# Kernel optimization log

Hardware: AMD Instinct MI355X
Metric: run time of the kernel (lower is better)

The kernel has to match this reference:

```python
import jax, jax.numpy as jnp
import numpy as np

EMBED = 1024
ATTN = 1024
HEADS = 16
HEAD_DIM = ATTN // HEADS


def setup_inputs() -> dict:
    key = jax.random.key(0)
    ks = jax.random.split(key, 8)
    s = 1.0 / np.sqrt(EMBED)
    sa = 1.0 / np.sqrt(ATTN)
    return {
        "queries": jax.random.normal(ks[0], (4, 512, EMBED), jnp.float32),
        "context": jax.random.normal(ks[1], (4, 2048, EMBED), jnp.float32),
        "Wq": jax.random.normal(ks[2], (EMBED, ATTN), jnp.float32) * s,
        "bq": jnp.zeros((ATTN,), jnp.float32),
        "Wkv": jax.random.normal(ks[3], (EMBED, 2 * ATTN), jnp.float32) * s,
        "bkv": jnp.zeros((2 * ATTN,), jnp.float32),
        "Wo": jax.random.normal(ks[4], (ATTN, EMBED), jnp.float32) * sa,
        "bo": jnp.zeros((EMBED,), jnp.float32),
    }


def reference(queries, context, Wq, bq, Wkv, bkv, Wo, bo):
    B, Lq, _ = queries.shape
    Lk = context.shape[1]
    q = queries @ Wq + bq                      # [B, Lq, ATTN]
    kv = context @ Wkv + bkv                   # [B, Lk, 2*ATTN]
    k, v = jnp.split(kv, 2, axis=-1)
    q = q.reshape(B, Lq, HEADS, HEAD_DIM)
    k = k.reshape(B, Lk, HEADS, HEAD_DIM)
    v = v.reshape(B, Lk, HEADS, HEAD_DIM)
    scale = 1.0 / np.sqrt(HEAD_DIM)
    scores = jnp.einsum("bqhd,bkhd->bhqk", q, k) * scale
    attn = jax.nn.softmax(scores, axis=-1)
    x = jnp.einsum("bhqk,bkhd->bqhd", attn, v).reshape(B, Lq, ATTN)
    return x @ Wo + bo
```

## Files before the change

### kernel.cpp

```cpp
#include <hip/hip_runtime.h>
#include <hip/hip_bf16.h>
#include <stdint.h>

typedef unsigned short u16;
typedef __attribute__((ext_vector_type(8))) __bf16 bf16x8;
typedef __attribute__((ext_vector_type(2))) __bf16 bf16x2;
typedef __attribute__((ext_vector_type(4))) float f32x4;
typedef __attribute__((ext_vector_type(4))) u16 u16x4;
typedef __attribute__((ext_vector_type(4))) float f32x4v;

typedef __attribute__((address_space(1))) void gvoid_t;
typedef __attribute__((address_space(3))) void lvoid_t;

#define BAR()    asm volatile("s_barrier" ::: "memory")
#define WAITV0() asm volatile("s_waitcnt vmcnt(0)" ::: "memory")
#define WAITV2() asm volatile("s_waitcnt vmcnt(2)" ::: "memory")
#define WAITV4() asm volatile("s_waitcnt vmcnt(4)" ::: "memory")
#define WAITV8() asm volatile("s_waitcnt vmcnt(8)" ::: "memory")

__device__ inline u16 f2bf(float f) {
    uint32_t u = __float_as_uint(f);
    u += 0x7fff + ((u >> 16) & 1);
    return (u16)(u >> 16);
}

__device__ inline float bf2f(u16 v) {
    return __uint_as_float(((uint32_t)v) << 16);
}

__device__ inline void gll16(const void* g, void* l) {
    __builtin_amdgcn_global_load_lds((gvoid_t*)g, (lvoid_t*)l, 16, 0, 0);
}

__device__ inline f32x4 mfma16(bf16x8 a, bf16x8 b, f32x4 c) {
    return __builtin_amdgcn_mfma_f32_16x16x32_bf16(a, b, c, 0, 0, 0);
}

__device__ inline int vslot(int r) {
    int n = r >> 4;
    return ((n >> 1) << 5) + (((r >> 2) & 3) << 3) + ((n & 1) << 2) + (r & 3);
}

__global__ __launch_bounds__(256) void prep_kernel(
        const float* __restrict__ q, const float* __restrict__ c,
        const float* __restrict__ Wq, const float* __restrict__ Wkv,
        const float* __restrict__ Wo, u16* __restrict__ qb,
        u16* __restrict__ cb, u16* __restrict__ WqT,
        u16* __restrict__ WkvT, u16* __restrict__ WoT) {
    const int bid = blockIdx.x;
    const int tid = threadIdx.x;
    if (bid < 10240) {
        int i = bid * 256 + tid;
        const float* src; u16* dst; int j;
        if (i < 524288) { src = q; dst = qb; j = i; }
        else            { src = c; dst = cb; j = i - 524288; }
        f32x4v f = ((const f32x4v*)src)[j];
        u16x4 o;
        o[0] = f2bf(f[0]); o[1] = f2bf(f[1]); o[2] = f2bf(f[2]); o[3] = f2bf(f[3]);
        ((u16x4*)dst)[j] = o;
        return;
    }
    int b2 = bid - 10240;
    const float* W; u16* WT; int N, n0, k0;
    if (b2 < 1024)      { W = Wq;  WT = WqT;  N = 1024; n0 = (b2 & 31) * 32; k0 = (b2 >> 5) * 32; }
    else if (b2 < 3072) { int b3 = b2 - 1024; W = Wkv; WT = WkvT; N = 2048; n0 = (b3 & 63) * 32; k0 = (b3 >> 6) * 32; }
    else                { int b3 = b2 - 3072; W = Wo;  WT = WoT;  N = 1024; n0 = (b3 & 31) * 32; k0 = (b3 >> 5) * 32; }
    __shared__ float t[32][33];
    int x = tid & 31, y = tid >> 5;
    for (int yy = y; yy < 32; yy += 8)
        t[yy][x] = W[(size_t)(k0 + yy) * N + n0 + x];
    __syncthreads();
    for (int yy = y; yy < 32; yy += 8)
        WT[(size_t)(n0 + yy) * 1024 + k0 + x] = f2bf(t[x][yy]);
}

template <int MODE>
__global__ __launch_bounds__(512, 2) void gemm_bt(
        const u16* __restrict__ A, const u16* __restrict__ Bt,
        const float* __restrict__ bias, int M, int N, int K,
        float scale, void* __restrict__ out0) {
    __shared__ u16 lds[4][6144];
    const int NT = K >> 5;
    const int tid = threadIdx.x;
    const int lane = tid & 63, wv = tid >> 6;
    const int c16 = lane & 15, g = lane >> 4;
    const int m0 = blockIdx.y * 64, n0 = blockIdx.x * 128;

    const int idxA = (wv & 3) * 64 + lane;
    const int rA = idxA >> 2, ccA = (idxA & 3) ^ ((rA >> 1) & 3);
    const size_t offA = (size_t)(m0 + rA) * K + ccA * 8;
    const int dstA = (wv & 3) * 512;
    const int idxB = wv * 64 + lane;
    const int rB = idxB >> 2, ccB = (idxB & 3) ^ ((rB >> 1) & 3);
    const size_t offB = (size_t)(n0 + rB) * K + ccB * 8;
    const int dstB = 2048 + wv * 512;

    auto stage = [&](int t) {
        gll16(A + offA + t * 32, &lds[t & 3][dstA]);
        gll16(Bt + offB + t * 32, &lds[t & 3][dstB]);
    };

    const int wm = (wv >> 1) * 16, wn = (wv & 1) * 64;
    f32x4 acc[4] = {};

    auto compute = [&](int slot) {
        const u16* la = &lds[slot][0];
        const u16* lb = &lds[slot][2048];
        int rowa = wm + c16;
        bf16x8 af = *(const bf16x8*)&la[rowa * 32 + (g ^ ((rowa >> 1) & 3)) * 8];
        bf16x8 bfr[4];
#pragma unroll
        for (int n = 0; n < 4; n++) {
            int row = wn + n * 16 + c16;
            bfr[n] = *(const bf16x8*)&lb[row * 32 + (g ^ ((row >> 1) & 3)) * 8];
        }
        __builtin_amdgcn_s_setprio(1);
#pragma unroll
        for (int n = 0; n < 4; n++)
            acc[n] = mfma16(af, bfr[n], acc[n]);
        __builtin_amdgcn_s_setprio(0);
    };

    stage(0); stage(1); stage(2);

    for (int t = 0; t < NT - 2; ++t) {
        WAITV4();
        BAR();
        if (t + 3 < NT) stage(t + 3);
        compute(t & 3);
    }
    WAITV2(); BAR(); compute((NT - 2) & 3);
    WAITV0(); BAR(); compute((NT - 1) & 3);

#pragma unroll
    for (int n = 0; n < 4; n++) {
        int col = n0 + wn + n * 16 + c16;
        float bv = bias[col];
        int rowb = m0 + wm + g * 4;
#pragma unroll
        for (int j = 0; j < 4; j++) {
            float v = (acc[n][j] + bv) * scale;
            int row = rowb + j;
            if (MODE == 0) {
                ((u16*)out0)[(size_t)row * N + col] = f2bf(v);
            } else {
                ((float*)out0)[(size_t)row * N + col] = v;
            }
        }
    }
}

__global__ __launch_bounds__(512, 2) void fused_qkv(
        const u16* __restrict__ cb, const u16* __restrict__ WkvT,
        const float* __restrict__ bkv, u16* __restrict__ Kp,
        u16* __restrict__ VpT,
        const u16* __restrict__ qb, const u16* __restrict__ WqT,
        const float* __restrict__ bq, float qscale, u16* __restrict__ Qp) {
    __shared__ u16 smem[4][2][8192];
    const int tid = threadIdx.x;
    const int lane = tid & 63, wv = tid >> 6;
    const int c16 = lane & 15, g = lane >> 4;
    const int bidg = blockIdx.x;

    if (bidg < 256) {
        const int K = 1024, NT = 32;
        const int cpx = 32;
        const int sw = (bidg & 7) * cpx + (bidg >> 3);
        const int bx = sw & 7, by = sw >> 3;
        const int m0 = by * 256, n0 = bx * 256;

        const int isB = wv >> 2;
        const int rbase = (wv & 3) * 64;
        const u16* src = isB ? WkvT : cb;
        const int base0 = isB ? n0 : m0;
        size_t off[4];
        const u16* ldst[4];
#pragma unroll
        for (int i = 0; i < 4; i++) {
            int rl = rbase + i * 16 + (lane >> 2);
            int ch = (lane & 3) ^ ((rl >> 1) & 3);
            off[i] = (size_t)(base0 + rl) * K + ch * 8;
            ldst[i] = &smem[0][0][0] + ((size_t)isB * 256 * 32) + (size_t)(rbase + i * 16) * 32;
        }
        const size_t slotStride = 2 * 256 * 32;

        auto stage = [&](int t) {
            const u16* s0 = src + (size_t)t * 32;
            u16* d = (u16*)ldst[0] + (size_t)(t & 3) * slotStride;
            gll16(s0 + off[0], d);
            gll16(s0 + off[1], d + 16 * 32);
            gll16(s0 + off[2], d + 32 * 32);
            gll16(s0 + off[3], d + 48 * 32);
        };

        const int wm = wv >> 2;
        const int wn = wv & 3;
        f32x4 acc[8][4] = {};

        auto compute = [&](int slot) {
            const u16* la = &smem[slot][0][0];
            const u16* lb = &smem[slot][1][0];
            bf16x8 af[8], bfr[4];
#pragma unroll
            for (int m = 0; m < 8; m++) {
                int row = wm * 128 + m * 16 + c16;
                af[m] = *(const bf16x8*)&la[row * 32 + (g ^ ((row >> 1) & 3)) * 8];
            }
#pragma unroll
            for (int n = 0; n < 4; n++) {
                int row = wn * 64 + n * 16 + c16;
                bfr[n] = *(const bf16x8*)&lb[row * 32 + (g ^ ((row >> 1) & 3)) * 8];
            }
            __builtin_amdgcn_s_setprio(1);
#pragma unroll
            for (int m = 0; m < 8; m++)
#pragma unroll
                for (int n = 0; n < 4; n++)
                    acc[m][n] = mfma16(af[m], bfr[n], acc[m][n]);
            __builtin_amdgcn_s_setprio(0);
        };

        stage(0); stage(1); stage(2);

        for (int t = 0; t < NT - 2; ++t) {
            WAITV8();
            BAR();
            if (t + 3 < NT) stage(t + 3);
            compute(t & 3);
        }
        WAITV4(); BAR(); compute((NT - 2) & 3);
        WAITV0(); BAR(); compute((NT - 1) & 3);

        const bool isV = (n0 >= 1024);
#pragma unroll
        for (int n = 0; n < 4; n++) {
            int col = n0 + wn * 64 + n * 16 + c16;
            float bv = bkv[col];
#pragma unroll
            for (int m = 0; m < 8; m++) {
                int rowb = m0 + wm * 128 + m * 16 + g * 4;
                if (isV) {
                    u16x4 pk;
#pragma unroll
                    for (int j = 0; j < 4; j++) pk[j] = f2bf(acc[m][n][j] + bv);
                    int vcol = (rowb & ~63) + vslot(rowb & 63);
                    *(u16x4*)&VpT[(size_t)(col - 1024) * 8192 + vcol] = pk;
                } else {
#pragma unroll
                    for (int j = 0; j < 4; j++)
                        Kp[(size_t)(rowb + j) * 1024 + col] = f2bf(acc[m][n][j] + bv);
                }
            }
        }
    } else {
        const int K = 1024, N = 1024, NT = 32;
        const int b2 = bidg - 256;
        const int m0 = (b2 >> 3) * 64, n0 = (b2 & 7) * 128;
        u16* base = &smem[0][0][0];

        const int idxA = (wv & 3) * 64 + lane;
        const int rA = idxA >> 2, ccA = (idxA & 3) ^ ((rA >> 1) & 3);
        const size_t offA = (size_t)(m0 + rA) * K + ccA * 8;
        const int dstA = (wv & 3) * 512;
        const int idxB = wv * 64 + lane;
        const int rB = idxB >> 2, ccB = (idxB & 3) ^ ((rB >> 1) & 3);
        const size_t offB = (size_t)(n0 + rB) * K + ccB * 8;
        const int dstB = 2048 + wv * 512;

        auto stage = [&](int t) {
            u16* d = base + (t & 3) * 6144;
            gll16(qb + offA + t * 32, d + dstA);
            gll16(WqT + offB + t * 32, d + dstB);
        };

        const int wm = (wv >> 1) * 16, wn = (wv & 1) * 64;
        f32x4 acc[4] = {};

        auto compute = [&](int slot) {
            const u16* la = base + slot * 6144;
            const u16* lb = la + 2048;
            int rowa = wm + c16;
            bf16x8 af = *(const bf16x8*)&la[rowa * 32 + (g ^ ((rowa >> 1) & 3)) * 8];
            bf16x8 bfr[4];
#pragma unroll
            for (int n = 0; n < 4; n++) {
                int row = wn + n * 16 + c16;
                bfr[n] = *(const bf16x8*)&lb[row * 32 + (g ^ ((row >> 1) & 3)) * 8];
            }
            __builtin_amdgcn_s_setprio(1);
#pragma unroll
            for (int n = 0; n < 4; n++)
                acc[n] = mfma16(af, bfr[n], acc[n]);
            __builtin_amdgcn_s_setprio(0);
        };

        stage(0); stage(1); stage(2);

        for (int t = 0; t < NT - 2; ++t) {
            WAITV4();
            BAR();
            if (t + 3 < NT) stage(t + 3);
            compute(t & 3);
        }
        WAITV2(); BAR(); compute((NT - 2) & 3);
        WAITV0(); BAR(); compute((NT - 1) & 3);

#pragma unroll
        for (int n = 0; n < 4; n++) {
            int col = n0 + wn + n * 16 + c16;
            float bv = bq[col];
            int rowb = m0 + wm + g * 4;
#pragma unroll
            for (int j = 0; j < 4; j++) {
                float v = (acc[n][j] + bv) * qscale;
                Qp[(size_t)(rowb + j) * N + col] = f2bf(v);
            }
        }
    }
}

__global__ __launch_bounds__(256, 3) void attn_split_kernel(
        const u16* __restrict__ Qp, const u16* __restrict__ Kp,
        const u16* __restrict__ VpT, u16* __restrict__ Opart,
        float* __restrict__ ml) {
    __shared__ u16 lKV[3][2][64 * 64];
    const int NT = 16;
    const int tid = threadIdx.x;
    const int lane = tid & 63, wv = tid >> 6;
    const int c16 = lane & 15, g = lane >> 4;
    const int bid = blockIdx.x;
    const int qblk = bid >> 7;
    const int low = bid & 127;
    const int h = low & 15, z = low >> 4;
    const int b = z >> 1, sp = z & 1;
    const int kvbase = sp * 1024;

    bf16x8 qf[2][2];
#pragma unroll
    for (int qs = 0; qs < 2; qs++) {
        int qrow = b * 512 + qblk * 128 + qs * 64 + wv * 16 + c16;
        qf[qs][0] = *(const bf16x8*)(Qp + (size_t)qrow * 1024 + h * 64 + g * 8);
        qf[qs][1] = *(const bf16x8*)(Qp + (size_t)qrow * 1024 + h * 64 + 32 + g * 8);
    }

    f32x4 acc[2][4] = {};
    float m_s[2] = {-1e30f, -1e30f}, l_s[2] = {0.f, 0.f};

    const int r0 = tid >> 3, c0 = (tid & 7) ^ (r0 & 7);
    const int r1 = 32 + r0,  c1 = (tid & 7) ^ (r1 & 7);
    const int dst0 = wv * 512, dst1 = 2048 + wv * 512;

    auto stageKV = [&](int t) {
        int slot = t % 3;
        int kv0 = kvbase + t * 64;
        u16* dK = &lKV[slot][0][0];
        u16* dV = &lKV[slot][1][0];
        gll16(Kp + (size_t)(b * 2048 + kv0 + r0) * 1024 + h * 64 + c0 * 8, dK + dst0);
        gll16(Kp + (size_t)(b * 2048 + kv0 + r1) * 1024 + h * 64 + c1 * 8, dK + dst1);
        gll16(VpT + (size_t)(h * 64 + r0) * 8192 + b * 2048 + kv0 + c0 * 8, dV + dst0);
        gll16(VpT + (size_t)(h * 64 + r1) * 8192 + b * 2048 + kv0 + c1 * 8, dV + dst1);
    };

    stageKV(0); stageKV(1);
    for (int t = 0; t < NT; ++t) {
        if (t < NT - 1) { WAITV4(); } else { WAITV0(); }
        BAR();
        if (t + 2 < NT) stageKV(t + 2);

        const int slot = t % 3;
        const u16* lK = &lKV[slot][0][0];
        const u16* lV = &lKV[slot][1][0];

        f32x4 s[2][4];
#pragma unroll
        for (int n = 0; n < 4; n++) {
            s[0][n] = f32x4{0.f, 0.f, 0.f, 0.f};
            s[1][n] = f32x4{0.f, 0.f, 0.f, 0.f};
        }
        __builtin_amdgcn_s_setprio(1);
#pragma unroll
        for (int n = 0; n < 4; n++) {
            int key = n * 16 + c16;
#pragma unroll
            for (int kk = 0; kk < 2; kk++) {
                bf16x8 kf = *(const bf16x8*)&lK[key * 64 + (((kk * 4 + g) ^ (key & 7))) * 8];
                s[0][n] = mfma16(kf, qf[0][kk], s[0][n]);
                s[1][n] = mfma16(kf, qf[1][kk], s[1][n]);
            }
        }
        __builtin_amdgcn_s_setprio(0);

        uint32_t r[2][4][2];
#pragma unroll
        for (int qs = 0; qs < 2; qs++) {
            float mn0 = fmaxf(fmaxf(s[qs][0][0], s[qs][0][1]), fmaxf(s[qs][0][2], s[qs][0][3]));
            float mn1 = fmaxf(fmaxf(s[qs][1][0], s[qs][1][1]), fmaxf(s[qs][1][2], s[qs][1][3]));
            float mn2 = fmaxf(fmaxf(s[qs][2][0], s[qs][2][1]), fmaxf(s[qs][2][2], s[qs][2][3]));
            float mn3 = fmaxf(fmaxf(s[qs][3][0], s[qs][3][1]), fmaxf(s[qs][3][2], s[qs][3][3]));
            float mx = fmaxf(fmaxf(mn0, mn1), fmaxf(mn2, mn3));
            mx = fmaxf(mx, __shfl_xor(mx, 16));
            mx = fmaxf(mx, __shfl_xor(mx, 32));

            if (!__all(mx - m_s[qs] <= 8.0f)) {
                float mn = fmaxf(m_s[qs], mx);
                float al = exp2f(m_s[qs] - mn);
                m_s[qs] = mn;
                l_s[qs] *= al;
                float alr[4];
#pragma unroll
                for (int j = 0; j < 4; j++) alr[j] = __shfl(al, g * 4 + j);
#pragma unroll
                for (int nd = 0; nd < 4; nd++)
#pragma unroll
                    for (int j = 0; j < 4; j++) acc[qs][nd][j] *= alr[j];
            }

            float sums[4];
#pragma unroll
            for (int n = 0; n < 4; n++) {
                float p0 = exp2f(s[qs][n][0] - m_s[qs]);
                float p1 = exp2f(s[qs][n][1] - m_s[qs]);
                float p2 = exp2f(s[qs][n][2] - m_s[qs]);
                float p3 = exp2f(s[qs][n][3] - m_s[qs]);
                sums[n] = (p0 + p1) + (p2 + p3);
                union { bf16x2 h; uint32_t u; } ca, cb;
                ca.h[0] = (__bf16)p0; ca.h[1] = (__bf16)p1;
                cb.h[0] = (__bf16)p2; cb.h[1] = (__bf16)p3;
                r[qs][n][0] = ca.u; r[qs][n][1] = cb.u;
            }
            float sum = (sums[0] + sums[1]) + (sums[2] + sums[3]);
            sum += __shfl_xor(sum, 16);
            sum += __shfl_xor(sum, 32);
            l_s[qs] += sum;
        }

        __builtin_amdgcn_s_setprio(1);
#pragma unroll
        for (int kk2 = 0; kk2 < 2; kk2++) {
            union { bf16x8 v8; uint32_t u[4]; } pa0, pa1;
            pa0.u[0] = r[0][kk2 * 2][0];     pa0.u[1] = r[0][kk2 * 2][1];
            pa0.u[2] = r[0][kk2 * 2 + 1][0]; pa0.u[3] = r[0][kk2 * 2 + 1][1];
            pa1.u[0] = r[1][kk2 * 2][0];     pa1.u[1] = r[1][kk2 * 2][1];
            pa1.u[2] = r[1][kk2 * 2 + 1][0]; pa1.u[3] = r[1][kk2 * 2 + 1][1];
#pragma unroll
            for (int nd = 0; nd < 4; nd++) {
                int d = nd * 16 + c16;
                bf16x8 vf = *(const bf16x8*)&lV[d * 64 + (((kk2 * 4 + g) ^ (d & 7))) * 8];
                acc[0][nd] = mfma16(pa0.v8, vf, acc[0][nd]);
                acc[1][nd] = mfma16(pa1.v8, vf, acc[1][nd]);
            }
        }
        __builtin_amdgcn_s_setprio(0);
    }

#pragma unroll
    for (int qs = 0; qs < 2; qs++) {
#pragma unroll
        for (int j = 0; j < 4; j++) {
            int rowq = b * 512 + qblk * 128 + qs * 64 + wv * 16 + g * 4 + j;
            size_t idx = (size_t)sp * 32768 + (size_t)rowq * 16 + h;
#pragma unroll
            for (int nd = 0; nd < 4; nd++)
                Opart[idx * 64 + nd * 16 + c16] = f2bf(acc[qs][nd][j]);
        }
        if (g == 0) {
            int rowq = b * 512 + qblk * 128 + qs * 64 + wv * 16 + c16;
            size_t idx = (size_t)sp * 32768 + (size_t)rowq * 16 + h;
            ml[idx * 2] = m_s[qs];
            ml[idx * 2 + 1] = l_s[qs];
        }
    }
}

__global__ __launch_bounds__(256) void attn_combine_kernel(
        const u16* __restrict__ Opart, const float* __restrict__ ml,
        u16* __restrict__ X) {
    const int tid = threadIdx.x;
    const int r = blockIdx.x * 4 + (tid >> 6);
    const int d = tid & 63;
    float m0 = ml[(size_t)r * 2], l0 = ml[(size_t)r * 2 + 1];
    float m1 = ml[(size_t)(32768 + r) * 2], l1 = ml[(size_t)(32768 + r) * 2 + 1];
    float M = fmaxf(m0, m1);
    float a0 = exp2f(m0 - M), a1 = exp2f(m1 - M);
    float li = 1.f / (l0 * a0 + l1 * a1);
    float o0 = bf2f(Opart[(size_t)r * 64 + d]);
    float o1 = bf2f(Opart[(size_t)(32768 + r) * 64 + d]);
    float o = (o0 * a0 + o1 * a1) * li;
    int qrow = r >> 4, h = r & 15;
    X[(size_t)qrow * 1024 + h * 64 + d] = f2bf(o);
}

extern "C" void kernel_launch(void* const* d_in, const int* in_sizes, int n_in,
                              void* d_out, int out_size, void* d_ws, size_t ws_size,
                              hipStream_t stream) {
    const float* queries = (const float*)d_in[0];
    const float* context = (const float*)d_in[1];
    const float* Wq      = (const float*)d_in[2];
    const float* bq      = (const float*)d_in[3];
    const float* Wkv     = (const float*)d_in[4];
    const float* bkv     = (const float*)d_in[5];
    const float* Wo      = (const float*)d_in[6];
    const float* bo      = (const float*)d_in[7];

    char* ws = (char*)d_ws;
    u16* qb   = (u16*)(ws);
    u16* cb   = (u16*)(ws + (4ull  << 20));
    u16* WqT  = (u16*)(ws + (20ull << 20));
    u16* WkvT = (u16*)(ws + (22ull << 20));
    u16* WoT  = (u16*)(ws + (26ull << 20));
    u16* Qp   = (u16*)(ws + (28ull << 20));
    u16* Kp   = (u16*)(ws + (32ull << 20));
    u16* VpT  = (u16*)(ws + (48ull << 20));
    u16* X    = (u16*)(ws + (64ull << 20));
    float* ml    = (float*)qb;
    u16*   Opart = (u16*)cb;

    prep_kernel<<<dim3(14336), dim3(256), 0, stream>>>(queries, context, Wq, Wkv, Wo,
                                                       qb, cb, WqT, WkvT, WoT);

    fused_qkv<<<dim3(512), dim3(512), 0, stream>>>(cb, WkvT, bkv, Kp, VpT,
                                                   qb, WqT, bq, 0.18033688f, Qp);
    attn_split_kernel<<<dim3(512), dim3(256), 0, stream>>>(Qp, Kp, VpT, Opart, ml);
    attn_combine_kernel<<<dim3(8192), dim3(256), 0, stream>>>(Opart, ml, X);
    gemm_bt<2><<<dim3(8, 32), dim3(512), 0, stream>>>(X, WoT, bo, 2048, 1024, 1024,
                                                      1.0f, d_out);
}
```

Baseline: 117.8 us.

## Fuse context fp32-to-bf16 conversion into KV projection GEMM loads

The separate prep pass that converted the fp32 context to bf16 is removed. The KV GEMM now reads fp32 context directly into registers, converts it to bf16 and writes it into LDS, while the weight tiles still use direct global-to-LDS loads. The pipeline is restructured with register double buffering (even/odd) and adjusted vmcnt/lgkmcnt waits. This saves a full write and re-read of the bf16 context buffer. In exchange the GEMM moves twice as many bytes for its A operand, uses more registers, and does conversion ALU work inside the main loop.

```diff
diff --git a/kernel.cpp b/kernel.cpp
--- a/kernel.cpp
+++ b/kernel.cpp
@@ -12,11 +12,14 @@
 typedef __attribute__((address_space(1))) void gvoid_t;
 typedef __attribute__((address_space(3))) void lvoid_t;
 
-#define BAR()    asm volatile("s_barrier" ::: "memory")
-#define WAITV0() asm volatile("s_waitcnt vmcnt(0)" ::: "memory")
-#define WAITV2() asm volatile("s_waitcnt vmcnt(2)" ::: "memory")
-#define WAITV4() asm volatile("s_waitcnt vmcnt(4)" ::: "memory")
-#define WAITV8() asm volatile("s_waitcnt vmcnt(8)" ::: "memory")
+#define BAR()     asm volatile("s_barrier" ::: "memory")
+#define WAITV0()  asm volatile("s_waitcnt vmcnt(0)" ::: "memory")
+#define WAITV2()  asm volatile("s_waitcnt vmcnt(2)" ::: "memory")
+#define WAITV4()  asm volatile("s_waitcnt vmcnt(4)" ::: "memory")
+#define WAITV6()  asm volatile("s_waitcnt vmcnt(6)" ::: "memory")
+#define WAITV8()  asm volatile("s_waitcnt vmcnt(8)" ::: "memory")
+#define WAITV12() asm volatile("s_waitcnt vmcnt(12)" ::: "memory")
+#define WAITLGKM0() asm volatile("s_waitcnt lgkmcnt(0)" ::: "memory")
 
 __device__ inline u16 f2bf(float f) {
     uint32_t u = __float_as_uint(f);
@@ -42,25 +45,21 @@
 }
 
 __global__ __launch_bounds__(256) void prep_kernel(
-        const float* __restrict__ q, const float* __restrict__ c,
-        const float* __restrict__ Wq, const float* __restrict__ Wkv,
-        const float* __restrict__ Wo, u16* __restrict__ qb,
-        u16* __restrict__ cb, u16* __restrict__ WqT,
+        const float* __restrict__ q, const float* __restrict__ Wq,
+        const float* __restrict__ Wkv, const float* __restrict__ Wo,
+        u16* __restrict__ qb, u16* __restrict__ WqT,
         u16* __restrict__ WkvT, u16* __restrict__ WoT) {
     const int bid = blockIdx.x;
     const int tid = threadIdx.x;
-    if (bid < 10240) {
+    if (bid < 2048) {
         int i = bid * 256 + tid;
-        const float* src; u16* dst; int j;
-        if (i < 524288) { src = q; dst = qb; j = i; }
-        else            { src = c; dst = cb; j = i - 524288; }
-        f32x4v f = ((const f32x4v*)src)[j];
+        f32x4v f = ((const f32x4v*)q)[i];
         u16x4 o;
         o[0] = f2bf(f[0]); o[1] = f2bf(f[1]); o[2] = f2bf(f[2]); o[3] = f2bf(f[3]);
-        ((u16x4*)dst)[j] = o;
+        ((u16x4*)qb)[i] = o;
         return;
     }
-    int b2 = bid - 10240;
+    int b2 = bid - 2048;
     const float* W; u16* WT; int N, n0, k0;
     if (b2 < 1024)      { W = Wq;  WT = WqT;  N = 1024; n0 = (b2 & 31) * 32; k0 = (b2 >> 5) * 32; }
     else if (b2 < 3072) { int b3 = b2 - 1024; W = Wkv; WT = WkvT; N = 2048; n0 = (b3 & 63) * 32; k0 = (b3 >> 6) * 32; }
@@ -151,7 +150,7 @@
 }
 
 __global__ __launch_bounds__(512, 2) void fused_qkv(
-        const u16* __restrict__ cb, const u16* __restrict__ WkvT,
+        const float* __restrict__ ctx, const u16* __restrict__ WkvT,
         const float* __restrict__ bkv, u16* __restrict__ Kp,
         u16* __restrict__ VpT,
         const u16* __restrict__ qb, const u16* __restrict__ WqT,
@@ -169,28 +168,42 @@
         const int bx = sw & 7, by = sw >> 3;
         const int m0 = by * 256, n0 = bx * 256;
 
-        const int isB = wv >> 2;
-        const int rbase = (wv & 3) * 64;
-        const u16* src = isB ? WkvT : cb;
-        const int base0 = isB ? n0 : m0;
-        size_t off[4];
-        const u16* ldst[4];
-#pragma unroll
-        for (int i = 0; i < 4; i++) {
-            int rl = rbase + i * 16 + (lane >> 2);
-            int ch = (lane & 3) ^ ((rl >> 1) & 3);
-            off[i] = (size_t)(base0 + rl) * K + ch * 8;
-            ldst[i] = &smem[0][0][0] + ((size_t)isB * 256 * 32) + (size_t)(rbase + i * 16) * 32;
-        }
-        const size_t slotStride = 2 * 256 * 32;
-
-        auto stage = [&](int t) {
-            const u16* s0 = src + (size_t)t * 32;
-            u16* d = (u16*)ldst[0] + (size_t)(t & 3) * slotStride;
-            gll16(s0 + off[0], d);
-            gll16(s0 + off[1], d + 16 * 32);
-            gll16(s0 + off[2], d + 32 * 32);
-            gll16(s0 + off[3], d + 48 * 32);
+        const int rA0 = tid >> 2,         chA0 = (tid & 3) ^ ((rA0 >> 1) & 3);
+        const int rA1 = (tid + 512) >> 2, chA1 = (tid & 3) ^ ((rA1 >> 1) & 3);
+        const size_t offA0 = (size_t)(m0 + rA0) * K + chA0 * 8;
+        const size_t offA1 = (size_t)(m0 + rA1) * K + chA1 * 8;
+        const int dA0 = tid * 8, dA1 = (tid + 512) * 8;
+        size_t offB[2]; int dstB[2];
+#pragma unroll
+        for (int j = 0; j < 2; j++) {
+            int cch = j * 512 + wv * 64 + lane;
+            int r = cch >> 2, ch = (cch & 3) ^ ((r >> 1) & 3);
+            offB[j] = (size_t)(n0 + r) * K + ch * 8;
+            dstB[j] = (j * 512 + wv * 64) * 8;
+        }
+
+        f32x4v raE[4], raO[4];
+        auto loadA = [&](int t, f32x4v* ra) {
+            ra[0] = *(const f32x4v*)(ctx + offA0 + (size_t)t * 32);
+            ra[1] = *(const f32x4v*)(ctx + offA0 + (size_t)t * 32 + 4);
+            ra[2] = *(const f32x4v*)(ctx + offA1 + (size_t)t * 32);
+            ra[3] = *(const f32x4v*)(ctx + offA1 + (size_t)t * 32 + 4);
+        };
+        auto writeA = [&](int t, const f32x4v* ra) {
+            u16* d = &smem[t & 3][0][0];
+            union { u16 s[8]; bf16x8 v; } p0, p1;
+#pragma unroll
+            for (int j = 0; j < 4; j++) {
+                p0.s[j] = f2bf(ra[0][j]); p0.s[4 + j] = f2bf(ra[1][j]);
+                p1.s[j] = f2bf(ra[2][j]); p1.s[4 + j] = f2bf(ra[3][j]);
+            }
+            *(bf16x8*)(d + dA0) = p0.v;
+            *(bf16x8*)(d + dA1) = p1.v;
+        };
+        auto stageB = [&](int t) {
+#pragma unroll
+            for (int j = 0; j < 2; j++)
+                gll16(WkvT + offB[j] + (size_t)t * 32, &smem[t & 3][1][0] + dstB[j]);
         };
 
         const int wm = wv >> 2;
@@ -220,16 +233,26 @@
             __builtin_amdgcn_s_setprio(0);
         };
 
-        stage(0); stage(1); stage(2);
-
-        for (int t = 0; t < NT - 2; ++t) {
-            WAITV8();
+        loadA(0, raE); stageB(0);
+        loadA(1, raO); stageB(1);
+        writeA(0, raE);
+        loadA(2, raE); stageB(2);
+        writeA(1, raO);
+
+        for (int t = 0; t < NT; ++t) {
+            if (t < NT - 2) { WAITV12(); } else if (t == NT - 2) { WAITV6(); } else { WAITV0(); }
+            WAITLGKM0();
             BAR();
-            if (t + 3 < NT) stage(t + 3);
+            if (t & 1) {
+                if (t + 3 < NT) loadA(t + 3, raE);
+                if (t + 2 < NT) writeA(t + 2, raO);
+            } else {
+                if (t + 3 < NT) loadA(t + 3, raO);
+                if (t + 2 < NT) writeA(t + 2, raE);
+            }
+            if (t + 3 < NT) stageB(t + 3);
             compute(t & 3);
         }
-        WAITV4(); BAR(); compute((NT - 2) & 3);
-        WAITV0(); BAR(); compute((NT - 1) & 3);
 
         const bool isV = (n0 >= 1024);
 #pragma unroll
@@ -504,7 +527,6 @@
 
     char* ws = (char*)d_ws;
     u16* qb   = (u16*)(ws);
-    u16* cb   = (u16*)(ws + (4ull  << 20));
     u16* WqT  = (u16*)(ws + (20ull << 20));
     u16* WkvT = (u16*)(ws + (22ull << 20));
     u16* WoT  = (u16*)(ws + (26ull << 20));
@@ -513,12 +535,12 @@
     u16* VpT  = (u16*)(ws + (48ull << 20));
     u16* X    = (u16*)(ws + (64ull << 20));
     float* ml    = (float*)qb;
-    u16*   Opart = (u16*)cb;
-
-    prep_kernel<<<dim3(14336), dim3(256), 0, stream>>>(queries, context, Wq, Wkv, Wo,
-                                                       qb, cb, WqT, WkvT, WoT);
-
-    fused_qkv<<<dim3(512), dim3(512), 0, stream>>>(cb, WkvT, bkv, Kp, VpT,
+    u16*   Opart = (u16*)(ws + (4ull << 20));
+
+    prep_kernel<<<dim3(6144), dim3(256), 0, stream>>>(queries, Wq, Wkv, Wo,
+                                                      qb, WqT, WkvT, WoT);
+
+    fused_qkv<<<dim3(512), dim3(512), 0, stream>>>(context, WkvT, bkv, Kp, VpT,
                                                    qb, WqT, bq, 0.18033688f, Qp);
     attn_split_kernel<<<dim3(512), dim3(256), 0, stream>>>(Qp, Kp, VpT, Opart, ml);
     attn_combine_kernel<<<dim3(8192), dim3(256), 0, stream>>>(Opart, ml, X);
```

Result: slower. 124.8 us (+5.9%).
